# Performance work log

Measured on AMD Instinct MI355X. Metric: run time of the kernel, lower is better.

## Reference

```python
import jax, jax.numpy as jnp
import numpy as np
from jax import lax

EPS = 1e-5

def layer_norm(x, g, b):
    m = x.mean(-1, keepdims=True)
    v = ((x - m) ** 2).mean(-1, keepdims=True)
    return (x - m) / jnp.sqrt(v + EPS) * g + b

def setup_inputs() -> dict:
    key = jax.random.key(0)
    ks = jax.random.split(key, 8)
    B, L, C = 8, 4096, 512
    latents = jax.random.normal(ks[0], (B, L, C), jnp.float32)
    dw_w = jax.random.normal(ks[1], (C, 1, 3), jnp.float32) * 0.02   # depthwise conv weight (O, I/g=1, K)
    dw_b = jnp.zeros((C,), jnp.float32)
    pw_w = jax.random.normal(ks[2], (C, C), jnp.float32) * 0.02      # pointwise (1x1) conv weight (out, in)
    pw_b = jnp.zeros((C,), jnp.float32)
    gate_w = jax.random.normal(ks[3], (2 * C,), jnp.float32) * 0.02  # mix_gate Linear(2C -> 1)
    gate_b = jnp.ones((), jnp.float32)                               # bias init to 1.0
    carrier_w = jax.random.normal(ks[4], (C,), jnp.float32) * 0.02   # carrier_score Linear(C -> 1)
    carrier_b = jnp.zeros((), jnp.float32)
    ln1_g = jnp.ones((C,), jnp.float32); ln1_b = jnp.zeros((C,), jnp.float32)
    ln2_g = jnp.ones((C,), jnp.float32); ln2_b = jnp.zeros((C,), jnp.float32)
    return {"latents": latents, "ln1_g": ln1_g, "ln1_b": ln1_b,
            "dw_w": dw_w, "dw_b": dw_b, "pw_w": pw_w, "pw_b": pw_b,
            "gate_w": gate_w, "gate_b": gate_b,
            "carrier_w": carrier_w, "carrier_b": carrier_b,
            "ln2_g": ln2_g, "ln2_b": ln2_b, "carrier_slots": 8}

def reference(latents, ln1_g, ln1_b, dw_w, dw_b, pw_w, pw_b,
              gate_w, gate_b, carrier_w, carrier_b, ln2_g, ln2_b, carrier_slots):
    B, L, C = latents.shape
    normalized = layer_norm(latents, ln1_g, ln1_b)          # [B, L, C]
    # depthwise conv1d: k=3, stride=2, pad=1, groups=C
    x = jnp.transpose(normalized, (0, 2, 1))                # [B, C, L]
    h = lax.conv_general_dilated(x, dw_w, window_strides=(2,), padding=[(1, 1)],
                                 feature_group_count=C,
                                 dimension_numbers=("NCH", "OIH", "NCH"))
    h = h + dw_b[None, :, None]
    h = jax.nn.gelu(h, approximate=False)                   # torch GELU default = exact erf
    reduced = jnp.einsum("oc,bcl->blo", pw_w, h) + pw_b     # pointwise 1x1 conv -> [B, Lr, C]
    # avg_pool1d(k=2, s=2, ceil_mode): L is even here so plain pairwise mean
    pooled = latents.reshape(B, L // 2, 2, C).mean(axis=2)  # [B, L/2, C]
    min_len = min(reduced.shape[1], pooled.shape[1])
    reduced = reduced[:, :min_len, :]
    pooled = pooled[:, :min_len, :]
    # gate on concat([reduced, pooled]) without materializing the concat
    logits = reduced @ gate_w[:C] + pooled @ gate_w[C:] + gate_b  # [B, min_len]
    gate = 0.5 + 0.5 * jax.nn.sigmoid(logits)[..., None]          # [B, min_len, 1]
    merged = pooled + gate * (reduced - pooled)
    if carrier_slots > 0 and L > carrier_slots:
        scores = normalized @ carrier_w + carrier_b          # [B, L]
        _, idx = lax.top_k(scores, carrier_slots)
        idx = jnp.sort(idx, axis=1)                          # [B, k]
        idx3 = jnp.broadcast_to(idx[:, :, None], (B, carrier_slots, C))
        carriers = jnp.take_along_axis(latents, idx3, axis=1)
        merged = jnp.concatenate([carriers, merged], axis=1)
    out = layer_norm(merged, ln2_g, ln2_b)                   # dropout p=0 (eval) -> identity
    return out, gate[..., 0]
```

## Files before the change

### kernel.cpp

```cpp
#include <hip/hip_runtime.h>
#include <hip/hip_bf16.h>
#include <math.h>

#define B_ 8
#define L_ 4096
#define C_ 512
#define LO_ 2048
#define SLOTS 8
#define LM_ 2056

typedef __attribute__((ext_vector_type(8))) short bf16x8;
typedef __attribute__((ext_vector_type(4))) float f32x4;
typedef unsigned short ushort_t;

__device__ __forceinline__ float waveReduceSum(float v){
  #pragma unroll
  for (int off = 32; off; off >>= 1) v += __shfl_xor(v, off);
  return v;
}

__device__ __forceinline__ unsigned short f2bf(float f){
  unsigned u = __float_as_uint(f);
  u += 0x7fffu + ((u >> 16) & 1u);
  return (unsigned short)(u >> 16);
}
__device__ __forceinline__ float bf2f(unsigned short b){
  return __uint_as_float(((unsigned)b) << 16);
}

#define GLOAD_LDS16(g, l) __builtin_amdgcn_global_load_lds( \
    (__attribute__((address_space(1))) void*)(g), \
    (__attribute__((address_space(3))) void*)(l), 16, 0, 0)

__global__ __launch_bounds__(256) void k_cast(const float* __restrict__ src, ushort_t* __restrict__ dst){
  int i = (blockIdx.x * 256 + threadIdx.x) * 4;
  float4 v = *(const float4*)(src + i);
  ushort4 o;
  o.x = f2bf(v.x); o.y = f2bf(v.y); o.z = f2bf(v.z); o.w = f2bf(v.w);
  *(ushort4*)(dst + i) = o;
}

__global__ __launch_bounds__(256) void k_conv(
    const float* __restrict__ lat, const float* __restrict__ g1, const float* __restrict__ b1,
    const float* __restrict__ dw, const float* __restrict__ db,
    const float* __restrict__ cw, const float* __restrict__ cbp,
    ushort_t* __restrict__ hbuf, ushort_t* __restrict__ pooled, float* __restrict__ scores)
{
  __shared__ float rows[9][C_];
  __shared__ float stat[9][3];
  __shared__ float sc_[2];
  int blk = blockIdx.x;
  int b = blk >> 9;
  int chunk = blk & 511;
  int t0 = chunk * 4;
  int tid = threadIdx.x;
  int wv = tid >> 6, lane = tid & 63;
  int lbase = 8 * chunk - 1;

  int c4 = lane * 4;
  float4 glo = *(const float4*)(g1 + c4);
  float4 ghi = *(const float4*)(g1 + 256 + c4);
  float4 wlo = *(const float4*)(cw + c4);
  float4 whi = *(const float4*)(cw + 256 + c4);
  float4 gclo, gchi;
  gclo.x = glo.x*wlo.x; gclo.y = glo.y*wlo.y; gclo.z = glo.z*wlo.z; gclo.w = glo.w*wlo.w;
  gchi.x = ghi.x*whi.x; gchi.y = ghi.y*whi.y; gchi.z = ghi.z*whi.z; gchi.w = ghi.w*whi.w;

  if (wv == 3){
    float4 blo = *(const float4*)(b1 + c4);
    float4 bhi = *(const float4*)(b1 + 256 + c4);
    float sgc = gclo.x+gclo.y+gclo.z+gclo.w + gchi.x+gchi.y+gchi.z+gchi.w;
    float sbc = blo.x*wlo.x + blo.y*wlo.y + blo.z*wlo.z + blo.w*wlo.w
              + bhi.x*whi.x + bhi.y*whi.y + bhi.z*whi.z + bhi.w*whi.w;
    sgc = waveReduceSum(sgc);
    sbc = waveReduceSum(sbc);
    if (lane == 0){ sc_[0] = sgc; sc_[1] = sbc; }
  }

  for (int r = wv; r < 9; r += 4){
    int l = lbase + r;
    float4 v0, v1;
    if (l >= 0){
      const float* xp = lat + ((size_t)(b * L_ + l)) * C_;
      v0 = *(const float4*)(xp + c4);
      v1 = *(const float4*)(xp + 256 + c4);
    } else {
      v0.x=0.f; v0.y=0.f; v0.z=0.f; v0.w=0.f;
      v1 = v0;
    }
    *(float4*)&rows[r][c4] = v0;
    *(float4*)&rows[r][256 + c4] = v1;
    float s1 = v0.x+v0.y+v0.z+v0.w + v1.x+v1.y+v1.z+v1.w;
    float s2 = v0.x*v0.x+v0.y*v0.y+v0.z*v0.z+v0.w*v0.w
             + v1.x*v1.x+v1.y*v1.y+v1.z*v1.z+v1.w*v1.w;
    float sd = v0.x*gclo.x+v0.y*gclo.y+v0.z*gclo.z+v0.w*gclo.w
             + v1.x*gchi.x+v1.y*gchi.y+v1.z*gchi.z+v1.w*gchi.w;
    s1 = waveReduceSum(s1);
    s2 = waveReduceSum(s2);
    sd = waveReduceSum(sd);
    if (lane == 0){
      float m = s1 * (1.f / C_);
      float var = s2 * (1.f / C_) - m * m;
      stat[r][0] = m;
      stat[r][1] = rsqrtf(var + 1e-5f);
      stat[r][2] = sd;
    }
  }
  __syncthreads();

  if (tid >= 1 && tid <= 8){
    int r = tid;
    float sc = (stat[r][2] - stat[r][0] * sc_[0]) * stat[r][1] + sc_[1] + cbp[0];
    scores[b * L_ + lbase + r] = sc;
  }

  int c = tid * 2;
  float g0 = g1[c], g1v = g1[c+1];
  float bb0 = b1[c], bb1 = b1[c+1];
  float w00 = dw[c*3+0], w01 = dw[c*3+1], w02 = dw[c*3+2];
  float w10 = dw[(c+1)*3+0], w11 = dw[(c+1)*3+1], w12 = dw[(c+1)*3+2];
  float db0 = db[c], db1 = db[c+1];
  float2 xr[9]; float mr[9], rr[9];
  #pragma unroll
  for (int r = 0; r < 9; r++){
    xr[r] = *(const float2*)&rows[r][c];
    mr[r] = stat[r][0]; rr[r] = stat[r][1];
  }
  bool pad0 = (chunk == 0);
  #pragma unroll
  for (int t = 0; t < 4; t++){
    int rl = 2*t, rm = 2*t+1, rrg = 2*t+2;
    float n0x, n0y;
    if (pad0 && t == 0){ n0x = 0.f; n0y = 0.f; }
    else {
      n0x = (xr[rl].x - mr[rl]) * rr[rl] * g0 + bb0;
      n0y = (xr[rl].y - mr[rl]) * rr[rl] * g1v + bb1;
    }
    float n1x = (xr[rm].x - mr[rm]) * rr[rm] * g0 + bb0;
    float n1y = (xr[rm].y - mr[rm]) * rr[rm] * g1v + bb1;
    float n2x = (xr[rrg].x - mr[rrg]) * rr[rrg] * g0 + bb0;
    float n2y = (xr[rrg].y - mr[rrg]) * rr[rrg] * g1v + bb1;
    float h0 = n0x * w00 + n1x * w01 + n2x * w02 + db0;
    float h1 = n0y * w10 + n1y * w11 + n2y * w12 + db1;
    float ge0 = 0.5f * h0 * (1.f + erff(h0 * 0.70710678118654752440f));
    float ge1 = 0.5f * h1 * (1.f + erff(h1 * 0.70710678118654752440f));
    size_t oidx = ((size_t)(b * LO_ + t0 + t)) * C_ + c;
    ushort2 hv; hv.x = f2bf(ge0); hv.y = f2bf(ge1);
    *(ushort2*)(hbuf + oidx) = hv;
    float p0 = 0.5f * (xr[rm].x + xr[rrg].x);
    float p1 = 0.5f * (xr[rm].y + xr[rrg].y);
    ushort2 pv; pv.x = f2bf(p0); pv.y = f2bf(p1);
    *(ushort2*)(pooled + oidx) = pv;
  }
}

__global__ __launch_bounds__(256) void k_topk1(
    const float* __restrict__ scores, float* __restrict__ cand_v, int* __restrict__ cand_i)
{
  __shared__ float sv[512];
  __shared__ float rv_[4];
  __shared__ int   ri_[4];
  int blk = blockIdx.x;
  int base = blk * 512;
  int tid = threadIdx.x;
  sv[tid] = scores[base + tid];
  sv[tid + 256] = scores[base + tid + 256];
  __syncthreads();
  int wv = tid >> 6, lane = tid & 63;
  for (int it = 0; it < SLOTS; it++){
    float v0 = sv[tid], v1 = sv[tid + 256];
    float best; int bi;
    if (v0 >= v1){ best = v0; bi = tid; } else { best = v1; bi = tid + 256; }
    #pragma unroll
    for (int off = 32; off; off >>= 1){
      float ov = __shfl_xor(best, off); int oi = __shfl_xor(bi, off);
      if (ov > best || (ov == best && oi < bi)){ best = ov; bi = oi; }
    }
    if (lane == 0){ rv_[wv] = best; ri_[wv] = bi; }
    __syncthreads();
    if (tid == 0){
      for (int w2 = 1; w2 < 4; w2++){
        if (rv_[w2] > best || (rv_[w2] == best && ri_[w2] < bi)){ best = rv_[w2]; bi = ri_[w2]; }
      }
      cand_v[blk * 8 + it] = best;
      cand_i[blk * 8 + it] = base + bi;
      sv[bi] = -INFINITY;
    }
    __syncthreads();
  }
}

__global__ __launch_bounds__(256) void k_topk2(
    const float* __restrict__ cand_v, const int* __restrict__ cand_i,
    const float* __restrict__ lat,
    const float* __restrict__ g2, const float* __restrict__ b2, float* __restrict__ out)
{
  __shared__ int chosen[SLOTS];
  int b = blockIdx.x, tid = threadIdx.x;
  if (tid < 64){
    float v = cand_v[b * 64 + tid];
    int  idx = cand_i[b * 64 + tid];
    for (int it = 0; it < SLOTS; it++){
      float best = v; int bi = idx;
      #pragma unroll
      for (int off = 32; off; off >>= 1){
        float ov = __shfl_xor(best, off); int oi = __shfl_xor(bi, off);
        if (ov > best || (ov == best && oi < bi)){ best = ov; bi = oi; }
      }
      if (tid == 0) chosen[it] = bi;
      if (idx == bi) v = -INFINITY;
    }
  }
  __syncthreads();
  if (tid == 0){
    for (int i = 0; i < SLOTS; i++)
      for (int j = i + 1; j < SLOTS; j++)
        if (chosen[j] < chosen[i]){ int t = chosen[i]; chosen[i] = chosen[j]; chosen[j] = t; }
  }
  __syncthreads();
  int wv = tid >> 6, lane = tid & 63;
  for (int s = wv; s < SLOTS; s += 4){
    int l = chosen[s] - b * L_;
    const float* x = lat + ((size_t)(b * L_ + l)) * C_;
    float xs[8];
    float s1 = 0.f, s2 = 0.f;
    #pragma unroll
    for (int i = 0; i < 2; i++){
      float4 vv = *(const float4*)(x + i * 256 + lane * 4);
      xs[i*4+0] = vv.x; xs[i*4+1] = vv.y; xs[i*4+2] = vv.z; xs[i*4+3] = vv.w;
      s1 += vv.x + vv.y + vv.z + vv.w;
      s2 += vv.x*vv.x + vv.y*vv.y + vv.z*vv.z + vv.w*vv.w;
    }
    s1 = waveReduceSum(s1); s2 = waveReduceSum(s2);
    float m = s1 * (1.f / C_);
    float rstd = rsqrtf(s2 * (1.f / C_) - m * m + 1e-5f);
    float* o = out + ((size_t)(b * LM_ + s)) * C_;
    #pragma unroll
    for (int i = 0; i < 2; i++){
      int cc = i * 256 + lane * 4;
      float4 gv = *(const float4*)(g2 + cc);
      float4 bv = *(const float4*)(b2 + cc);
      float4 ov;
      ov.x = (xs[i*4+0] - m) * rstd * gv.x + bv.x;
      ov.y = (xs[i*4+1] - m) * rstd * gv.y + bv.y;
      ov.z = (xs[i*4+2] - m) * rstd * gv.z + bv.z;
      ov.w = (xs[i*4+3] - m) * rstd * gv.w + bv.w;
      *(float4*)(o + cc) = ov;
    }
  }
}

__global__ __launch_bounds__(256) void k_gemm(
    const ushort_t* __restrict__ A, const ushort_t* __restrict__ Bw,
    const float* __restrict__ bias, ushort_t* __restrict__ Cout)
{
  __shared__ short As[2][128][32];
  __shared__ short Bs[2][128][32];
  int tid = threadIdx.x;
  int w = tid >> 6, lane = tid & 63;
  int row0 = blockIdx.y * 128, col0 = blockIdx.x * 128;
  int wr = (w >> 1) * 64, wc = (w & 1) * 64;
  int srow = lane >> 2;
  int scol = (lane & 3) * 8;
  int fr = lane & 15, kq = (lane >> 4) * 8;

  f32x4 acc[4][4];
  #pragma unroll
  for (int m = 0; m < 4; m++)
    #pragma unroll
    for (int n = 0; n < 4; n++)
      acc[m][n] = (f32x4){0.f, 0.f, 0.f, 0.f};

  #pragma unroll
  for (int j = 0; j < 2; j++){
    int i = 2*w + j;
    GLOAD_LDS16(A  + (size_t)(row0 + 16*i + srow) * C_ + scol, &As[0][16*i][0]);
    GLOAD_LDS16(Bw + (size_t)(col0 + 16*i + srow) * C_ + scol, &Bs[0][16*i][0]);
  }
  __syncthreads();

  int cur = 0;
  for (int kt = 0; kt < 16; kt++){
    if (kt < 15){
      int k0n = (kt + 1) * 32;
      #pragma unroll
      for (int j = 0; j < 2; j++){
        int i = 2*w + j;
        GLOAD_LDS16(A  + (size_t)(row0 + 16*i + srow) * C_ + k0n + scol, &As[cur^1][16*i][0]);
        GLOAD_LDS16(Bw + (size_t)(col0 + 16*i + srow) * C_ + k0n + scol, &Bs[cur^1][16*i][0]);
      }
    }
    bf16x8 af[4], bfr[4];
    #pragma unroll
    for (int m = 0; m < 4; m++) af[m]  = *(const bf16x8*)&As[cur][wr + m*16 + fr][kq];
    #pragma unroll
    for (int n = 0; n < 4; n++) bfr[n] = *(const bf16x8*)&Bs[cur][wc + n*16 + fr][kq];
    #pragma unroll
    for (int m = 0; m < 4; m++)
      #pragma unroll
      for (int n = 0; n < 4; n++)
        acc[m][n] = __builtin_amdgcn_mfma_f32_16x16x32_bf16(af[m], bfr[n], acc[m][n], 0, 0, 0);
    __syncthreads();
    cur ^= 1;
  }

  int cq = lane & 15, rq = (lane >> 4) * 4;
  #pragma unroll
  for (int n = 0; n < 4; n++){
    int col = col0 + wc + n*16 + cq;
    float bv = bias[col];
    #pragma unroll
    for (int m = 0; m < 4; m++){
      #pragma unroll
      for (int j = 0; j < 4; j++){
        int row = row0 + wr + m*16 + rq + j;
        Cout[(size_t)row * C_ + col] = f2bf(acc[m][n][j] + bv);
      }
    }
  }
}

__global__ __launch_bounds__(256) void k_epilogue(
    const ushort_t* __restrict__ red, const ushort_t* __restrict__ pooled,
    const float* __restrict__ gw, const float* __restrict__ gbp,
    const float* __restrict__ g2, const float* __restrict__ b2,
    float* __restrict__ out, float* __restrict__ gateout)
{
  int row  = blockIdx.x * 4 + (threadIdx.x >> 6);
  int lane = threadIdx.x & 63;
  int b = row >> 11, l = row & (LO_ - 1);
  const ushort_t* rr = red + (size_t)row * C_;
  const ushort_t* pp = pooled + (size_t)row * C_;
  float rv[8], pv[8];
  float lp = 0.f;
  #pragma unroll
  for (int i = 0; i < 2; i++){
    int c = i * 256 + lane * 4;
    ushort4 r4 = *(const ushort4*)(rr + c);
    ushort4 p4 = *(const ushort4*)(pp + c);
    float4 w1 = *(const float4*)(gw + c);
    float4 w2 = *(const float4*)(gw + C_ + c);
    float r0 = bf2f(r4.x), r1 = bf2f(r4.y), r2 = bf2f(r4.z), r3 = bf2f(r4.w);
    float q0 = bf2f(p4.x), q1 = bf2f(p4.y), q2 = bf2f(p4.z), q3 = bf2f(p4.w);
    rv[i*4+0] = r0; rv[i*4+1] = r1; rv[i*4+2] = r2; rv[i*4+3] = r3;
    pv[i*4+0] = q0; pv[i*4+1] = q1; pv[i*4+2] = q2; pv[i*4+3] = q3;
    lp += r0*w1.x + r1*w1.y + r2*w1.z + r3*w1.w
        + q0*w2.x + q1*w2.y + q2*w2.z + q3*w2.w;
  }
  lp = waveReduceSum(lp);
  float gate = 0.5f + 0.5f / (1.f + expf(-(lp + gbp[0])));
  float mv[8];
  float s1 = 0.f, s2 = 0.f;
  #pragma unroll
  for (int j = 0; j < 8; j++){
    mv[j] = pv[j] + gate * (rv[j] - pv[j]);
    s1 += mv[j]; s2 += mv[j] * mv[j];
  }
  s1 = waveReduceSum(s1); s2 = waveReduceSum(s2);
  float m = s1 * (1.f / C_);
  float rstd = rsqrtf(s2 * (1.f / C_) - m * m + 1e-5f);
  float* o = out + ((size_t)(b * LM_ + SLOTS + l)) * C_;
  #pragma unroll
  for (int i = 0; i < 2; i++){
    int c = i * 256 + lane * 4;
    float4 gv = *(const float4*)(g2 + c);
    float4 bv = *(const float4*)(b2 + c);
    float4 ov;
    ov.x = (mv[i*4+0] - m) * rstd * gv.x + bv.x;
    ov.y = (mv[i*4+1] - m) * rstd * gv.y + bv.y;
    ov.z = (mv[i*4+2] - m) * rstd * gv.z + bv.z;
    ov.w = (mv[i*4+3] - m) * rstd * gv.w + bv.w;
    *(float4*)(o + c) = ov;
  }
  if (lane == 0) gateout[b * LO_ + l] = gate;
}

extern "C" void kernel_launch(void* const* d_in, const int* in_sizes, int n_in,
                              void* d_out, int out_size, void* d_ws, size_t ws_size,
                              hipStream_t stream)
{
  const float* lat = (const float*)d_in[0];
  const float* g1  = (const float*)d_in[1];
  const float* b1  = (const float*)d_in[2];
  const float* dw  = (const float*)d_in[3];
  const float* db  = (const float*)d_in[4];
  const float* pw  = (const float*)d_in[5];
  const float* pb  = (const float*)d_in[6];
  const float* gw  = (const float*)d_in[7];
  const float* gb  = (const float*)d_in[8];
  const float* cw  = (const float*)d_in[9];
  const float* cb  = (const float*)d_in[10];
  const float* g2  = (const float*)d_in[11];
  const float* b2  = (const float*)d_in[12];

  float* out = (float*)d_out;
  float* gateout = out + (size_t)B_ * LM_ * C_;

  const size_t NHL = (size_t)B_ * LO_ * C_;
  ushort_t* hbuf   = (ushort_t*)d_ws;
  ushort_t* pooled = hbuf + NHL;
  ushort_t* redb   = pooled + NHL;
  ushort_t* pwb    = redb + NHL;
  float*    scores = (float*)(pwb + (size_t)C_ * C_);
  float*    cand_v = scores + (size_t)B_ * L_;
  int*      cand_i = (int*)(cand_v + B_ * 64);

  hipLaunchKernelGGL(k_cast,    dim3(C_ * C_ / 1024), dim3(256), 0, stream, pw, pwb);
  hipLaunchKernelGGL(k_conv,    dim3(B_ * LO_ / 4), dim3(256), 0, stream,
                     lat, g1, b1, dw, db, cw, cb, hbuf, pooled, scores);
  hipLaunchKernelGGL(k_topk1,   dim3(B_ * 8), dim3(256), 0, stream, scores, cand_v, cand_i);
  hipLaunchKernelGGL(k_topk2,   dim3(B_), dim3(256), 0, stream, cand_v, cand_i, lat, g2, b2, out);
  hipLaunchKernelGGL(k_gemm,    dim3(C_ / 128, B_ * LO_ / 128), dim3(256), 0, stream, hbuf, pwb, pb, redb);
  hipLaunchKernelGGL(k_epilogue,dim3(B_ * LO_ / 4), dim3(256), 0, stream, redb, pooled, gw, gb, g2, b2, out, gateout);
}
```

Before: 77.17 us.

## Fold weight cast into conv, merge top-k kernels, enlarge conv tiles, swizzle GEMM

Moves the pointwise weight bf16 cast into the conv kernel's first 256 blocks, which removes one launch. Doubles the conv tile to 8 outputs per block with 512 threads, so fewer halo rows are reloaded, and vectorises channel work to 4-wide. Replaces the two-stage top-k with a single 1024-thread kernel per batch, removing a launch and the global candidate buffers. Also remaps GEMM block indices so blocks that run together spread across row tiles; the cost is a fully serial 8-iteration top-k on only 8 blocks.

Measured after the change: 75.96 us. No clear change (-1.6%).

```diff
diff --git a/kernel.cpp b/kernel.cpp
--- a/kernel.cpp
+++ b/kernel.cpp
@@ -32,30 +32,30 @@
     (__attribute__((address_space(1))) void*)(g), \
     (__attribute__((address_space(3))) void*)(l), 16, 0, 0)
 
-__global__ __launch_bounds__(256) void k_cast(const float* __restrict__ src, ushort_t* __restrict__ dst){
-  int i = (blockIdx.x * 256 + threadIdx.x) * 4;
-  float4 v = *(const float4*)(src + i);
-  ushort4 o;
-  o.x = f2bf(v.x); o.y = f2bf(v.y); o.z = f2bf(v.z); o.w = f2bf(v.w);
-  *(ushort4*)(dst + i) = o;
-}
-
-__global__ __launch_bounds__(256) void k_conv(
+__global__ __launch_bounds__(512) void k_conv(
     const float* __restrict__ lat, const float* __restrict__ g1, const float* __restrict__ b1,
     const float* __restrict__ dw, const float* __restrict__ db,
     const float* __restrict__ cw, const float* __restrict__ cbp,
+    const float* __restrict__ pw, ushort_t* __restrict__ pwb,
     ushort_t* __restrict__ hbuf, ushort_t* __restrict__ pooled, float* __restrict__ scores)
 {
-  __shared__ float rows[9][C_];
-  __shared__ float stat[9][3];
+  __shared__ float rows[17][C_];
+  __shared__ float stat[17][3];
   __shared__ float sc_[2];
   int blk = blockIdx.x;
-  int b = blk >> 9;
-  int chunk = blk & 511;
-  int t0 = chunk * 4;
+  int b = blk >> 8;
+  int chunk = blk & 255;
+  int t0 = chunk * 8;
   int tid = threadIdx.x;
   int wv = tid >> 6, lane = tid & 63;
-  int lbase = 8 * chunk - 1;
+  int lbase = 16 * chunk - 1;
+
+  if (blk < 256){
+    int i = blk * 1024 + tid * 2;
+    float2 v = *(const float2*)(pw + i);
+    ushort2 o; o.x = f2bf(v.x); o.y = f2bf(v.y);
+    *(ushort2*)(pwb + i) = o;
+  }
 
   int c4 = lane * 4;
   float4 glo = *(const float4*)(g1 + c4);
@@ -66,7 +66,7 @@
   gclo.x = glo.x*wlo.x; gclo.y = glo.y*wlo.y; gclo.z = glo.z*wlo.z; gclo.w = glo.w*wlo.w;
   gchi.x = ghi.x*whi.x; gchi.y = ghi.y*whi.y; gchi.z = ghi.z*whi.z; gchi.w = ghi.w*whi.w;
 
-  if (wv == 3){
+  if (wv == 7){
     float4 blo = *(const float4*)(b1 + c4);
     float4 bhi = *(const float4*)(b1 + 256 + c4);
     float sgc = gclo.x+gclo.y+gclo.z+gclo.w + gchi.x+gchi.y+gchi.z+gchi.w;
@@ -77,7 +77,7 @@
     if (lane == 0){ sc_[0] = sgc; sc_[1] = sbc; }
   }
 
-  for (int r = wv; r < 9; r += 4){
+  for (int r = wv; r < 17; r += 8){
     int l = lbase + r;
     float4 v0, v1;
     if (l >= 0){
@@ -108,69 +108,79 @@
   }
   __syncthreads();
 
-  if (tid >= 1 && tid <= 8){
+  if (tid >= 1 && tid <= 16){
     int r = tid;
     float sc = (stat[r][2] - stat[r][0] * sc_[0]) * stat[r][1] + sc_[1] + cbp[0];
     scores[b * L_ + lbase + r] = sc;
   }
 
-  int c = tid * 2;
-  float g0 = g1[c], g1v = g1[c+1];
-  float bb0 = b1[c], bb1 = b1[c+1];
-  float w00 = dw[c*3+0], w01 = dw[c*3+1], w02 = dw[c*3+2];
-  float w10 = dw[(c+1)*3+0], w11 = dw[(c+1)*3+1], w12 = dw[(c+1)*3+2];
-  float db0 = db[c], db1 = db[c+1];
-  float2 xr[9]; float mr[9], rr[9];
-  #pragma unroll
-  for (int r = 0; r < 9; r++){
-    xr[r] = *(const float2*)&rows[r][c];
-    mr[r] = stat[r][0]; rr[r] = stat[r][1];
-  }
-  bool pad0 = (chunk == 0);
-  #pragma unroll
-  for (int t = 0; t < 4; t++){
+  int th = tid >> 7;
+  int cq = (tid & 127) * 4;
+  float4 gq = *(const float4*)(g1 + cq);
+  float4 bq = *(const float4*)(b1 + cq);
+  float4 dbq = *(const float4*)(db + cq);
+  float4 w0 = *(const float4*)(dw + cq*3);
+  float4 w1 = *(const float4*)(dw + cq*3 + 4);
+  float4 w2 = *(const float4*)(dw + cq*3 + 8);
+  float wk[4][3] = {{w0.x, w0.y, w0.z}, {w0.w, w1.x, w1.y},
+                    {w1.z, w1.w, w2.x}, {w2.y, w2.z, w2.w}};
+  float gk[4] = {gq.x, gq.y, gq.z, gq.w};
+  float bk[4] = {bq.x, bq.y, bq.z, bq.w};
+  float dbk[4] = {dbq.x, dbq.y, dbq.z, dbq.w};
+  #pragma unroll
+  for (int i = 0; i < 2; i++){
+    int t = th * 2 + i;
     int rl = 2*t, rm = 2*t+1, rrg = 2*t+2;
-    float n0x, n0y;
-    if (pad0 && t == 0){ n0x = 0.f; n0y = 0.f; }
-    else {
-      n0x = (xr[rl].x - mr[rl]) * rr[rl] * g0 + bb0;
-      n0y = (xr[rl].y - mr[rl]) * rr[rl] * g1v + bb1;
-    }
-    float n1x = (xr[rm].x - mr[rm]) * rr[rm] * g0 + bb0;
-    float n1y = (xr[rm].y - mr[rm]) * rr[rm] * g1v + bb1;
-    float n2x = (xr[rrg].x - mr[rrg]) * rr[rrg] * g0 + bb0;
-    float n2y = (xr[rrg].y - mr[rrg]) * rr[rrg] * g1v + bb1;
-    float h0 = n0x * w00 + n1x * w01 + n2x * w02 + db0;
-    float h1 = n0y * w10 + n1y * w11 + n2y * w12 + db1;
-    float ge0 = 0.5f * h0 * (1.f + erff(h0 * 0.70710678118654752440f));
-    float ge1 = 0.5f * h1 * (1.f + erff(h1 * 0.70710678118654752440f));
-    size_t oidx = ((size_t)(b * LO_ + t0 + t)) * C_ + c;
-    ushort2 hv; hv.x = f2bf(ge0); hv.y = f2bf(ge1);
-    *(ushort2*)(hbuf + oidx) = hv;
-    float p0 = 0.5f * (xr[rm].x + xr[rrg].x);
-    float p1 = 0.5f * (xr[rm].y + xr[rrg].y);
-    ushort2 pv; pv.x = f2bf(p0); pv.y = f2bf(p1);
-    *(ushort2*)(pooled + oidx) = pv;
-  }
-}
-
-__global__ __launch_bounds__(256) void k_topk1(
-    const float* __restrict__ scores, float* __restrict__ cand_v, int* __restrict__ cand_i)
-{
-  __shared__ float sv[512];
-  __shared__ float rv_[4];
-  __shared__ int   ri_[4];
-  int blk = blockIdx.x;
-  int base = blk * 512;
-  int tid = threadIdx.x;
-  sv[tid] = scores[base + tid];
-  sv[tid + 256] = scores[base + tid + 256];
+    float4 xl = *(const float4*)&rows[rl][cq];
+    float4 xm = *(const float4*)&rows[rm][cq];
+    float4 xrr = *(const float4*)&rows[rrg][cq];
+    float ml = stat[rl][0], rlr = stat[rl][1];
+    float mm = stat[rm][0], rmr = stat[rm][1];
+    float mr2 = stat[rrg][0], rrr = stat[rrg][1];
+    bool zpad = (chunk == 0 && t == 0);
+    float xlv[4] = {xl.x, xl.y, xl.z, xl.w};
+    float xmv[4] = {xm.x, xm.y, xm.z, xm.w};
+    float xrv[4] = {xrr.x, xrr.y, xrr.z, xrr.w};
+    ushort4 hv, pv;
+    unsigned short* hp = (unsigned short*)&hv;
+    unsigned short* pp = (unsigned short*)&pv;
+    #pragma unroll
+    for (int k = 0; k < 4; k++){
+      float n0 = zpad ? 0.f : ((xlv[k] - ml) * rlr * gk[k] + bk[k]);
+      float n1 = (xmv[k] - mm) * rmr * gk[k] + bk[k];
+      float n2 = (xrv[k] - mr2) * rrr * gk[k] + bk[k];
+      float hh = n0 * wk[k][0] + n1 * wk[k][1] + n2 * wk[k][2] + dbk[k];
+      float ge = 0.5f * hh * (1.f + erff(hh * 0.70710678118654752440f));
+      hp[k] = f2bf(ge);
+      pp[k] = f2bf(0.5f * (xmv[k] + xrv[k]));
+    }
+    size_t oidx = ((size_t)(b * LO_ + t0 + t)) * C_ + cq;
+    *(ushort4*)(hbuf + oidx) = hv;
+    *(ushort4*)(pooled + oidx) = pv;
+  }
+}
+
+__global__ __launch_bounds__(1024) void k_topk(
+    const float* __restrict__ scores, const float* __restrict__ lat,
+    const float* __restrict__ g2, const float* __restrict__ b2, float* __restrict__ out)
+{
+  __shared__ float sv[L_];
+  __shared__ float rv_[16];
+  __shared__ int   ri_[16];
+  __shared__ int   chosen[SLOTS];
+  int b = blockIdx.x, tid = threadIdx.x;
+  #pragma unroll
+  for (int j = 0; j < 4; j++) sv[tid + j * 1024] = scores[b * L_ + tid + j * 1024];
   __syncthreads();
   int wv = tid >> 6, lane = tid & 63;
   for (int it = 0; it < SLOTS; it++){
-    float v0 = sv[tid], v1 = sv[tid + 256];
-    float best; int bi;
-    if (v0 >= v1){ best = v0; bi = tid; } else { best = v1; bi = tid + 256; }
+    float best = -INFINITY; int bi = L_;
+    #pragma unroll
+    for (int j = 0; j < 4; j++){
+      int i = tid + j * 1024;
+      float v = sv[i];
+      if (v > best || (v == best && i < bi)){ best = v; bi = i; }
+    }
     #pragma unroll
     for (int off = 32; off; off >>= 1){
       float ov = __shfl_xor(best, off); int oi = __shfl_xor(bi, off);
@@ -179,48 +189,23 @@
     if (lane == 0){ rv_[wv] = best; ri_[wv] = bi; }
     __syncthreads();
     if (tid == 0){
-      for (int w2 = 1; w2 < 4; w2++){
+      for (int w2 = 1; w2 < 16; w2++){
         if (rv_[w2] > best || (rv_[w2] == best && ri_[w2] < bi)){ best = rv_[w2]; bi = ri_[w2]; }
       }
-      cand_v[blk * 8 + it] = best;
-      cand_i[blk * 8 + it] = base + bi;
+      chosen[it] = bi;
       sv[bi] = -INFINITY;
     }
     __syncthreads();
   }
-}
-
-__global__ __launch_bounds__(256) void k_topk2(
-    const float* __restrict__ cand_v, const int* __restrict__ cand_i,
-    const float* __restrict__ lat,
-    const float* __restrict__ g2, const float* __restrict__ b2, float* __restrict__ out)
-{
-  __shared__ int chosen[SLOTS];
-  int b = blockIdx.x, tid = threadIdx.x;
-  if (tid < 64){
-    float v = cand_v[b * 64 + tid];
-    int  idx = cand_i[b * 64 + tid];
-    for (int it = 0; it < SLOTS; it++){
-      float best = v; int bi = idx;
-      #pragma unroll
-      for (int off = 32; off; off >>= 1){
-        float ov = __shfl_xor(best, off); int oi = __shfl_xor(bi, off);
-        if (ov > best || (ov == best && oi < bi)){ best = ov; bi = oi; }
-      }
-      if (tid == 0) chosen[it] = bi;
-      if (idx == bi) v = -INFINITY;
-    }
-  }
-  __syncthreads();
   if (tid == 0){
     for (int i = 0; i < SLOTS; i++)
       for (int j = i + 1; j < SLOTS; j++)
         if (chosen[j] < chosen[i]){ int t = chosen[i]; chosen[i] = chosen[j]; chosen[j] = t; }
   }
   __syncthreads();
-  int wv = tid >> 6, lane = tid & 63;
-  for (int s = wv; s < SLOTS; s += 4){
-    int l = chosen[s] - b * L_;
+  if (wv < SLOTS){
+    int s = wv;
+    int l = chosen[s];
     const float* x = lat + ((size_t)(b * L_ + l)) * C_;
     float xs[8];
     float s1 = 0.f, s2 = 0.f;
@@ -258,7 +243,9 @@
   __shared__ short Bs[2][128][32];
   int tid = threadIdx.x;
   int w = tid >> 6, lane = tid & 63;
-  int row0 = blockIdx.y * 128, col0 = blockIdx.x * 128;
+  int hw = blockIdx.y * 4 + blockIdx.x;
+  int tile = ((hw & 7) << 6) | (hw >> 3);
+  int row0 = (tile >> 2) * 128, col0 = (tile & 3) * 128;
   int wr = (w >> 1) * 64, wc = (w & 1) * 64;
   int srow = lane >> 2;
   int scol = (lane & 3) * 8;
@@ -402,14 +389,10 @@
   ushort_t* redb   = pooled + NHL;
   ushort_t* pwb    = redb + NHL;
   float*    scores = (float*)(pwb + (size_t)C_ * C_);
-  float*    cand_v = scores + (size_t)B_ * L_;
-  int*      cand_i = (int*)(cand_v + B_ * 64);
-
-  hipLaunchKernelGGL(k_cast,    dim3(C_ * C_ / 1024), dim3(256), 0, stream, pw, pwb);
-  hipLaunchKernelGGL(k_conv,    dim3(B_ * LO_ / 4), dim3(256), 0, stream,
-                     lat, g1, b1, dw, db, cw, cb, hbuf, pooled, scores);
-  hipLaunchKernelGGL(k_topk1,   dim3(B_ * 8), dim3(256), 0, stream, scores, cand_v, cand_i);
-  hipLaunchKernelGGL(k_topk2,   dim3(B_), dim3(256), 0, stream, cand_v, cand_i, lat, g2, b2, out);
-  hipLaunchKernelGGL(k_gemm,    dim3(C_ / 128, B_ * LO_ / 128), dim3(256), 0, stream, hbuf, pwb, pb, redb);
+
+  hipLaunchKernelGGL(k_conv,    dim3(B_ * LO_ / 8), dim3(512), 0, stream,
+                     lat, g1, b1, dw, db, cw, cb, pw, pwb, hbuf, pooled, scores);
+  hipLaunchKernelGGL(k_topk,    dim3(B_), dim3(1024), 0, stream, scores, lat, g2, b2, out);
+  hipLaunchKernelGGL(k_gemm,    dim3(4, 128), dim3(256), 0, stream, hbuf, pwb, pb, redb);
   hipLaunchKernelGGL(k_epilogue,dim3(B_ * LO_ / 4), dim3(256), 0, stream, redb, pooled, gw, gb, g2, b2, out, gateout);
 }
```
